# Kernel tuning notes

Hardware: AMD Instinct MI355X
Metric: run time of the kernel (lower is better)

Reference implementation:

```python
import jax, jax.numpy as jnp
import numpy as np

D = 256
H = 4
L = 6
N = 32768
NH = N // H  # 8192 per-head width
VOCAB = 256
B, T = 1, 1024
ROPE_BASE = 10000.0


def ln(x):
    # LayerNorm over last dim, no affine (elementwise_affine=False)
    m = jnp.mean(x, axis=-1, keepdims=True)
    v = jnp.var(x, axis=-1, keepdims=True)
    return (x - m) * jax.lax.rsqrt(v + 1e-5)


def rope(x):
    # standard rotary position embedding over the last dim (split-half convention)
    Dh = x.shape[-1]
    t = x.shape[-2]
    half = Dh // 2
    inv_freq = 1.0 / (ROPE_BASE ** (jnp.arange(half, dtype=jnp.float32) / half))
    ang = jnp.arange(t, dtype=jnp.float32)[:, None] * inv_freq[None, :]  # [T, half]
    cos, sin = jnp.cos(ang), jnp.sin(ang)
    x1, x2 = x[..., :half], x[..., half:]
    return jnp.concatenate([x1 * cos - x2 * sin, x2 * cos + x1 * sin], axis=-1)


def setup_inputs() -> dict:
    key = jax.random.key(0)
    ks = jax.random.split(key, 6)
    std = 0.02
    return {
        "idx": jax.random.randint(ks[0], (B, T), 0, VOCAB, dtype=jnp.int32),
        "wte": std * jax.random.normal(ks[1], (VOCAB, D), dtype=jnp.float32),
        "encoder": std * jax.random.normal(ks[2], (N, D), dtype=jnp.float32),
        "decoder_x": std * jax.random.normal(ks[3], (H, D, NH), dtype=jnp.float32),
        "decoder_y": std * jax.random.normal(ks[4], (H, D, NH), dtype=jnp.float32),
        "readout": std * jax.random.normal(ks[5], (D, VOCAB), dtype=jnp.float32),
    }


def reference(idx, wte, encoder, decoder_x, decoder_y, readout):
    b, t = idx.shape
    v = ln(wte[idx])  # [B, T, D]
    # strict causal mask (tril with diagonal=-1): position i attends to j < i
    mask = jnp.tril(jnp.ones((t, t), dtype=bool), k=-1)
    for _ in range(L):
        # x: relu(v @ decoder_x) -> [B, H, T, NH]
        x = jax.nn.relu(jnp.einsum('btd,hdn->bhtn', v, decoder_x))
        xr = rope(x)  # Q = K = x
        # unnormalized causal linear attention, strict lower triangular
        scores = jnp.einsum('bhtn,bhsn->bhts', xr, xr)
        scores = jnp.where(mask, scores, 0.0)
        a = jnp.einsum('bhts,bsd->bhtd', scores, v)  # V = v (broadcast over heads)
        # gated wide projection
        y = jax.nn.relu(jnp.einsum('bhtd,hdn->bhtn', ln(a), decoder_y)) * x
        # [B,H,T,NH] -> [B,T,H*NH] = [B,T,N]  (matches transpose(1,2).reshape)
        y = jnp.transpose(y, (0, 2, 1, 3)).reshape(b, t, N)
        v = ln(v + ln(y @ encoder))  # dropout is identity in eval
    return v @ readout  # [B, T, VOCAB]
```

## Files before the change

kernel.cpp:

```cpp
#include <hip/hip_runtime.h>
#include <hip/hip_bf16.h>
#include <stdint.h>

typedef unsigned short u16;
typedef unsigned int u32;
typedef __attribute__((ext_vector_type(8))) short i16x8;
typedef __attribute__((ext_vector_type(4))) float f32x4;

#define DEV __device__ __forceinline__

constexpr int T = 1024, D = 256, H = 4, NH = 8192, NF = 32768, HALF = 4096;

constexpr size_t OFF_DXT  = 0;
constexpr size_t OFF_DYT  = OFF_DXT  + (size_t)H*NH*D*2;
constexpr size_t OFF_ENCT = OFF_DYT  + (size_t)H*NH*D*2;
constexpr size_t OFF_ROT  = OFF_ENCT + (size_t)D*NF*2;
constexpr size_t OFF_COS  = OFF_ROT  + (size_t)D*D*2;
constexpr size_t OFF_SIN  = OFF_COS  + (size_t)T*HALF*4;
constexpr size_t OFF_V    = OFF_SIN  + (size_t)T*HALF*4;
constexpr size_t OFF_VBF  = OFF_V    + (size_t)T*D*4;
constexpr size_t OFF_VT   = OFF_VBF  + (size_t)T*D*2;
constexpr size_t OFF_X    = OFF_VT   + (size_t)T*D*2;
constexpr size_t OFF_XR   = OFF_X    + (size_t)T*NF*2;
constexpr size_t OFF_SC   = OFF_XR   + (size_t)T*NF*2;
constexpr size_t OFF_LA   = OFF_SC   + (size_t)H*T*T*2;
constexpr size_t OFF_PART = OFF_LA   + (size_t)H*T*D*2;
constexpr size_t WS_NEED  = OFF_PART + (size_t)8*T*T*4;


DEV u16 f2bf(float f) {
  u32 u = __float_as_uint(f);
  u += 0x7FFFu + ((u >> 16) & 1u);
  return (u16)(u >> 16);
}
DEV float bf2f(u16 u) { return __uint_as_float(((u32)u) << 16); }

DEV float2 block_sum2(float a, float b, float* sb) {
  #pragma unroll
  for (int o = 32; o > 0; o >>= 1) {
    a += __shfl_down(a, o, 64);
    b += __shfl_down(b, o, 64);
  }
  const int w = threadIdx.x >> 6;
  __syncthreads();
  if ((threadIdx.x & 63) == 0) { sb[w*2] = a; sb[w*2+1] = b; }
  __syncthreads();
  return make_float2(sb[0]+sb[2]+sb[4]+sb[6], sb[1]+sb[3]+sb[5]+sb[7]);
}

DEV void stage128(const u16* __restrict__ g, int ld, char* lds, int wave, int lane) {
  #pragma unroll
  for (int i = 0; i < 4; ++i) {
    const int f = (wave*4 + i)*64 + lane;
    const int row = f >> 3, seg = f & 7;
    const int segl = seg ^ (row & 7);
    const u16* src = g + (size_t)row*ld + segl*8;
    __builtin_amdgcn_global_load_lds(
        (const __attribute__((address_space(1))) void*)src,
        (__attribute__((address_space(3))) void*)(lds + ((wave*4 + i) << 10)),
        16, 0, 0);
  }
}

DEV void gemm_bt_core(const u16* __restrict__ Ab, int lda,
                      const u16* __restrict__ Bb, int ldb,
                      int nkt, char* smem, f32x4 acc[4][4]) {
  const int tid = threadIdx.x, lane = tid & 63, wave = tid >> 6;
  const int wm = wave >> 1, wn = wave & 1;
  const int lr = lane & 15, lk = lane >> 4;
  char* As = smem;
  char* Bs = smem + 32768;
  #pragma unroll
  for (int m = 0; m < 4; ++m)
    #pragma unroll
    for (int n = 0; n < 4; ++n) acc[m][n] = f32x4{0.f, 0.f, 0.f, 0.f};
  stage128(Ab, lda, As, wave, lane);
  stage128(Bb, ldb, Bs, wave, lane);
  __syncthreads();
  for (int kt = 0; kt < nkt; ++kt) {
    const int cur = kt & 1;
    if (kt + 1 < nkt) {
      stage128(Ab + (size_t)(kt+1)*64, lda, As + ((cur^1) << 14), wave, lane);
      stage128(Bb + (size_t)(kt+1)*64, ldb, Bs + ((cur^1) << 14), wave, lane);
    }
    const char* Ac = As + (cur << 14);
    const char* Bc = Bs + (cur << 14);
    #pragma unroll
    for (int kk = 0; kk < 2; ++kk) {
      const int lcol = kk*64 + lk*16;
      i16x8 af[4], bfv[4];
      #pragma unroll
      for (int m = 0; m < 4; ++m) {
        const int row = wm*64 + m*16 + lr;
        af[m] = *(const i16x8*)(Ac + row*128 + (lcol ^ ((row & 7) << 4)));
      }
      #pragma unroll
      for (int n = 0; n < 4; ++n) {
        const int row = wn*64 + n*16 + lr;
        bfv[n] = *(const i16x8*)(Bc + row*128 + (lcol ^ ((row & 7) << 4)));
      }
      #pragma unroll
      for (int m = 0; m < 4; ++m)
        #pragma unroll
        for (int n = 0; n < 4; ++n)
          acc[m][n] = __builtin_amdgcn_mfma_f32_16x16x32_bf16(af[m], bfv[n], acc[m][n], 0, 0, 0);
    }
    __syncthreads();
  }
}

#define EPILOG_IDX() \
  const int lane = threadIdx.x & 63, wave = threadIdx.x >> 6; \
  const int wm = wave >> 1, wn = wave & 1, lr = lane & 15, lk = lane >> 4; \
  const int r0 = wm*64 + lk*4; \
  const int c0 = wn*64 + lr;

constexpr int TS = 136;
template<int MODE>
DEV void store_tile(const f32x4 acc[4][4], u16* __restrict__ dst, int ld,
                    const u16* __restrict__ xg, char* smem) {
  u16* tb = (u16*)smem;
  EPILOG_IDX();
  #pragma unroll
  for (int m = 0; m < 4; ++m)
    #pragma unroll
    for (int n = 0; n < 4; ++n)
      #pragma unroll
      for (int r = 0; r < 4; ++r) {
        float v = acc[m][n][r];
        if (MODE >= 1) v = fmaxf(v, 0.f);
        tb[(size_t)(r0 + m*16 + r)*TS + c0 + n*16] = f2bf(v);
      }
  __syncthreads();
  const int rr = threadIdx.x >> 4;
  const int cc = (threadIdx.x & 15)*8;
  #pragma unroll
  for (int it = 0; it < 8; ++it) {
    const int row = it*16 + rr;
    i16x8 w = *(const i16x8*)(tb + (size_t)row*TS + cc);
    if (MODE == 2) {
      const i16x8 xv = *(const i16x8*)(xg + (size_t)row*ld + cc);
      #pragma unroll
      for (int j = 0; j < 8; ++j)
        w[j] = (short)f2bf(bf2f((u16)w[j]) * bf2f((u16)xv[j]));
    }
    *(i16x8*)(dst + (size_t)row*ld + cc) = w;
  }
}

template<int PERM>
__global__ __launch_bounds__(256) void k_transpose_cvt(const float* __restrict__ in,
                                                       u16* __restrict__ out, int R, int C) {
  __shared__ float tile[32][33];
  const size_t zoff = (size_t)blockIdx.z * R * C;
  const float* inz = in + zoff;
  u16* outz = out + zoff;
  const int c0 = blockIdx.x << 5, rr0 = blockIdx.y << 5;
  const int tx = threadIdx.x & 31, ty = threadIdx.x >> 5;
  #pragma unroll
  for (int i = 0; i < 4; ++i) {
    int irow = rr0 + ty + i*8;
    if (PERM == 2) {
      const int hh = irow >> 13, j = irow & 8191;
      irow = hh*8192 + ((j & 1) ? (j >> 1) + 4096 : (j >> 1));
    }
    tile[ty + i*8][tx] = inz[(size_t)irow*C + c0 + tx];
  }
  __syncthreads();
  #pragma unroll
  for (int i = 0; i < 4; ++i) {
    const int rr = ty + i*8;
    int orow = c0 + rr;
    if (PERM == 1) {
      const int j = orow & 8191;
      orow = (orow & ~8191) | ((j < 4096) ? 2*j : 2*(j - 4096) + 1);
    }
    outz[(size_t)orow*R + rr0 + tx] = f2bf(tile[tx][rr]);
  }
}

__global__ __launch_bounds__(256) void k_rope_table(float* __restrict__ cosT,
                                                    float* __restrict__ sinT) {
  const int i = blockIdx.x*256 + threadIdx.x;
  const int t = blockIdx.y;
  const float p = (float)i * (1.f/4096.f);
  const float ang = (float)t * expf(-9.210340371976184f * p);
  cosT[(size_t)t*HALF + i] = cosf(ang);
  sinT[(size_t)t*HALF + i] = sinf(ang);
}

__global__ __launch_bounds__(256) void k_embed(const int* __restrict__ idx,
                                               const float* __restrict__ wte,
                                               float* __restrict__ v,
                                               u16* __restrict__ vbf, u16* __restrict__ vT) {
  __shared__ float sb[8];
  const int t = blockIdx.x, d = threadIdx.x;
  const float val = wte[(size_t)idx[t]*D + d];
  float2 ss = block_sum2(val, val*val, sb);
  const float m = ss.x*(1.f/256.f), var = ss.y*(1.f/256.f) - m*m;
  const float vn = (val - m) * rsqrtf(var + 1e-5f);
  v[(size_t)t*D + d] = vn;
  const u16 b = f2bf(vn);
  vbf[(size_t)t*D + d] = b;
  vT[(size_t)d*T + t] = b;
}

__global__ __launch_bounds__(256) void k_gemm_x_rope(const u16* __restrict__ vbf,
                                                     const u16* __restrict__ dxT,
                                                     u16* __restrict__ x,
                                                     u16* __restrict__ xr,
                                                     const float* __restrict__ cosT,
                                                     const float* __restrict__ sinT) {
  __shared__ char smem[65536];
  const int nt = blockIdx.x, mt = blockIdx.y, h = blockIdx.z;
  f32x4 acc[4][4];
  gemm_bt_core(vbf + (size_t)mt*128*D, D,
               dxT + ((size_t)h*NH + (size_t)nt*128)*D, D, 4, smem, acc);
  u16* tb = (u16*)smem;
  {
    EPILOG_IDX();
    #pragma unroll
    for (int m = 0; m < 4; ++m)
      #pragma unroll
      for (int n = 0; n < 4; ++n)
        #pragma unroll
        for (int r = 0; r < 4; ++r)
          tb[(size_t)(r0 + m*16 + r)*TS + c0 + n*16] = f2bf(fmaxf(acc[m][n][r], 0.f));
  }
  __syncthreads();
  const int rr = threadIdx.x >> 4;
  const int cc = (threadIdx.x & 15)*8;
  const size_t obase = (size_t)mt*128*NF + (size_t)h*NH + (size_t)nt*128;
  const int pbase = (nt*128 + cc) >> 1;
  #pragma unroll
  for (int it = 0; it < 8; ++it) {
    const int row = it*16 + rr;
    const i16x8 w = *(const i16x8*)(tb + (size_t)row*TS + cc);
    *(i16x8*)(x + obase + (size_t)row*NF + cc) = w;
    const int t = mt*128 + row;
    const float4 cv = *(const float4*)(cosT + (size_t)t*HALF + pbase);
    const float4 sv = *(const float4*)(sinT + (size_t)t*HALF + pbase);
    i16x8 r;
    float x1, x2;
    x1 = bf2f((u16)w[0]); x2 = bf2f((u16)w[1]);
    r[0] = (short)f2bf(x1*cv.x - x2*sv.x); r[1] = (short)f2bf(x2*cv.x + x1*sv.x);
    x1 = bf2f((u16)w[2]); x2 = bf2f((u16)w[3]);
    r[2] = (short)f2bf(x1*cv.y - x2*sv.y); r[3] = (short)f2bf(x2*cv.y + x1*sv.y);
    x1 = bf2f((u16)w[4]); x2 = bf2f((u16)w[5]);
    r[4] = (short)f2bf(x1*cv.z - x2*sv.z); r[5] = (short)f2bf(x2*cv.z + x1*sv.z);
    x1 = bf2f((u16)w[6]); x2 = bf2f((u16)w[7]);
    r[6] = (short)f2bf(x1*cv.w - x2*sv.w); r[7] = (short)f2bf(x2*cv.w + x1*sv.w);
    *(i16x8*)(xr + obase + (size_t)row*NF + cc) = r;
  }
}

__global__ __launch_bounds__(256) void k_gemm_sc(const u16* __restrict__ xr,
                                                 u16* __restrict__ scb) {
  __shared__ char smem[65536];
  const int z = blockIdx.x & 15;
  const int i = blockIdx.x >> 4;
  int tt = 0;
  while ((tt + 1)*(tt + 2)/2 <= i) ++tt;
  const int st = i - tt*(tt + 1)/2;
  const int h = z >> 2, kc = z & 3;
  const u16* base = xr + (size_t)h*NH + (size_t)kc*2048;
  f32x4 acc[4][4];
  gemm_bt_core(base + (size_t)tt*128*NF, NF, base + (size_t)st*128*NF, NF, 32, smem, acc);
  store_tile<0>(acc, scb + (size_t)z*T*T + (size_t)tt*128*T + (size_t)st*128, T,
                nullptr, smem);
}

__global__ __launch_bounds__(256) void k_sc_combine(const u16* __restrict__ scb,
                                                    u16* __restrict__ sc) {
  const int row = blockIdx.x;
  const int h = row >> 10, t = row & 1023;
  const u16* p0 = scb + ((size_t)(h*4 + 0)*T + t)*T;
  u16* o = sc + (size_t)row*T;
  const int s0 = threadIdx.x*4;
  ushort4 r;
  if (s0 >= t) {
    r.x = 0; r.y = 0; r.z = 0; r.w = 0;
  } else {
    const ushort4 a0 = *(const ushort4*)(p0 + s0);
    const ushort4 a1 = *(const ushort4*)(p0 + T*T + s0);
    const ushort4 a2 = *(const ushort4*)(p0 + 2*(size_t)T*T + s0);
    const ushort4 a3 = *(const ushort4*)(p0 + 3*(size_t)T*T + s0);
    const float vx = bf2f(a0.x) + bf2f(a1.x) + bf2f(a2.x) + bf2f(a3.x);
    const float vy = bf2f(a0.y) + bf2f(a1.y) + bf2f(a2.y) + bf2f(a3.y);
    const float vz = bf2f(a0.z) + bf2f(a1.z) + bf2f(a2.z) + bf2f(a3.z);
    const float vw = bf2f(a0.w) + bf2f(a1.w) + bf2f(a2.w) + bf2f(a3.w);
    r.x = f2bf((s0 + 0 < t) ? vx : 0.f);
    r.y = f2bf((s0 + 1 < t) ? vy : 0.f);
    r.z = f2bf((s0 + 2 < t) ? vz : 0.f);
    r.w = f2bf((s0 + 3 < t) ? vw : 0.f);
  }
  *(ushort4*)(o + s0) = r;
}

__global__ __launch_bounds__(256) void k_gemm_av(const u16* __restrict__ sc,
                                                 const u16* __restrict__ vT,
                                                 float* __restrict__ part) {
  __shared__ char smem[65536];
  const int slot = blockIdx.x & 7;
  const int h = slot >> 1, nt = slot & 1;
  int mt = 0, kc = 0, rem = blockIdx.x >> 3;
  #pragma unroll
  for (int m = 0; m < 8; ++m) {
    const int c = (m >> 1) + 1;
    if (rem < c) { mt = m; kc = rem; break; }
    rem -= c;
  }
  f32x4 acc[4][4];
  gemm_bt_core(sc + ((size_t)h*T + (size_t)mt*128)*T + (size_t)kc*256, T,
               vT + (size_t)nt*128*T + (size_t)kc*256, T, 4, smem, acc);
  EPILOG_IDX();
  float* Cp = part + (size_t)(h*4 + kc) * T * D;
  const int tb = mt*128 + r0, cb = nt*128 + c0;
  #pragma unroll
  for (int m = 0; m < 4; ++m)
    #pragma unroll
    for (int n = 0; n < 4; ++n)
      #pragma unroll
      for (int r = 0; r < 4; ++r)
        Cp[(size_t)(tb + m*16 + r)*D + cb + n*16] = acc[m][n][r];
}

__global__ __launch_bounds__(256) void k_ln_a(const float* __restrict__ part,
                                              u16* __restrict__ la) {
  __shared__ float sb[8];
  const int row = blockIdx.x;
  const int h = row >> 10, t = row & 1023;
  const int d = threadIdx.x;
  const int nkc = ((t >> 7) >> 1) + 1;
  float s = 0.f;
  for (int kc = 0; kc < nkc; ++kc)
    s += part[((size_t)(h*4 + kc)*T + t)*D + d];
  float2 ss = block_sum2(s, s*s, sb);
  const float m = ss.x*(1.f/256.f), var = ss.y*(1.f/256.f) - m*m;
  la[(size_t)row*D + d] = f2bf((s - m) * rsqrtf(var + 1e-5f));
}

__global__ __launch_bounds__(256) void k_gemm_y(const u16* __restrict__ la,
                                                const u16* __restrict__ dyT,
                                                const u16* __restrict__ x,
                                                u16* __restrict__ y) {
  __shared__ char smem[65536];
  const int nt = blockIdx.x, mt = blockIdx.y, h = blockIdx.z;
  f32x4 acc[4][4];
  gemm_bt_core(la + ((size_t)h*T + (size_t)mt*128)*D, D,
               dyT + ((size_t)h*NH + (size_t)nt*128)*D, D, 4, smem, acc);
  const size_t off = (size_t)mt*128*NF + (size_t)h*NH + (size_t)nt*128;
  store_tile<2>(acc, y + off, NF, x + off, smem);
}

__global__ __launch_bounds__(256) void k_gemm_enc(const u16* __restrict__ y,
                                                  const u16* __restrict__ encT,
                                                  float* __restrict__ part) {
  __shared__ char smem[65536];
  const int slot = blockIdx.x & 7;
  const int seq  = blockIdx.x >> 3;
  const int kcc = slot*4 + (seq >> 4);
  const int nt = seq & 1;
  const int mt = (seq >> 1) & 7;
  f32x4 acc[4][4];
  gemm_bt_core(y + (size_t)mt*128*NF + (size_t)kcc*1024, NF,
               encT + (size_t)nt*128*NF + (size_t)kcc*1024, NF, 16, smem, acc);
  EPILOG_IDX();
  float* Cp = part + (size_t)kcc * T * D;
  const int tb = mt*128 + r0, cb = nt*128 + c0;
  #pragma unroll
  for (int m = 0; m < 4; ++m)
    #pragma unroll
    for (int n = 0; n < 4; ++n)
      #pragma unroll
      for (int r = 0; r < 4; ++r)
        Cp[(size_t)(tb + m*16 + r)*D + cb + n*16] = acc[m][n][r];
}

__global__ __launch_bounds__(256) void k_newv(const float* __restrict__ part,
                                              float* __restrict__ v,
                                              u16* __restrict__ vbf, u16* __restrict__ vT) {
  __shared__ float sb[8];
  const int t = blockIdx.x, d = threadIdx.x;
  float s = 0.f;
  #pragma unroll
  for (int kc = 0; kc < 32; ++kc)
    s += part[((size_t)kc*T + t)*D + d];
  float2 ss = block_sum2(s, s*s, sb);
  float m = ss.x*(1.f/256.f), var = ss.y*(1.f/256.f) - m*m;
  const float l1 = (s - m) * rsqrtf(var + 1e-5f);
  const float u = v[(size_t)t*D + d] + l1;
  float2 s2 = block_sum2(u, u*u, sb);
  m = s2.x*(1.f/256.f); var = s2.y*(1.f/256.f) - m*m;
  const float vn = (u - m) * rsqrtf(var + 1e-5f);
  v[(size_t)t*D + d] = vn;
  const u16 bb = f2bf(vn);
  vbf[(size_t)t*D + d] = bb;
  vT[(size_t)d*T + t] = bb;
}

__global__ __launch_bounds__(256) void k_gemm_out(const u16* __restrict__ vbf,
                                                  const u16* __restrict__ roT,
                                                  float* __restrict__ out) {
  __shared__ char smem[65536];
  const int nt = blockIdx.x, mt = blockIdx.y;
  f32x4 acc[4][4];
  gemm_bt_core(vbf + (size_t)mt*128*D, D, roT + (size_t)nt*128*D, D, 4, smem, acc);
  EPILOG_IDX();
  const int tb = mt*128 + r0, cb = nt*128 + c0;
  #pragma unroll
  for (int m = 0; m < 4; ++m)
    #pragma unroll
    for (int n = 0; n < 4; ++n)
      #pragma unroll
      for (int r = 0; r < 4; ++r)
        out[(size_t)(tb + m*16 + r)*D + cb + n*16] = acc[m][n][r];
}

extern "C" void kernel_launch(void* const* d_in, const int* in_sizes, int n_in,
                              void* d_out, int out_size, void* d_ws, size_t ws_size,
                              hipStream_t stream) {
  (void)in_sizes; (void)n_in; (void)out_size; (void)ws_size;
  const int*   idx = (const int*)d_in[0];
  const float* wte = (const float*)d_in[1];
  const float* enc = (const float*)d_in[2];
  const float* dx  = (const float*)d_in[3];
  const float* dy  = (const float*)d_in[4];
  const float* ro  = (const float*)d_in[5];
  float* out = (float*)d_out;
  char* ws = (char*)d_ws;

  u16* dxT  = (u16*)(ws + OFF_DXT);
  u16* dyT  = (u16*)(ws + OFF_DYT);
  u16* encT = (u16*)(ws + OFF_ENCT);
  u16* roT  = (u16*)(ws + OFF_ROT);
  float* cosT = (float*)(ws + OFF_COS);
  float* sinT = (float*)(ws + OFF_SIN);
  float* v    = (float*)(ws + OFF_V);
  u16* vbf  = (u16*)(ws + OFF_VBF);
  u16* vT   = (u16*)(ws + OFF_VT);
  u16* x    = (u16*)(ws + OFF_X);
  u16* xr   = (u16*)(ws + OFF_XR);
  u16* sc   = (u16*)(ws + OFF_SC);
  u16* la   = (u16*)(ws + OFF_LA);
  u16* scb  = (u16*)(ws + OFF_PART);
  float* part = (float*)(ws + OFF_PART);

  k_transpose_cvt<1><<<dim3(NH/32, D/32, H), 256, 0, stream>>>(dx, dxT, D, NH);
  k_transpose_cvt<1><<<dim3(NH/32, D/32, H), 256, 0, stream>>>(dy, dyT, D, NH);
  k_transpose_cvt<2><<<dim3(D/32, NF/32, 1), 256, 0, stream>>>(enc, encT, NF, D);
  k_transpose_cvt<0><<<dim3(D/32, D/32, 1), 256, 0, stream>>>(ro, roT, D, D);
  k_rope_table<<<dim3(HALF/256, T), 256, 0, stream>>>(cosT, sinT);
  k_embed<<<T, 256, 0, stream>>>(idx, wte, v, vbf, vT);

  for (int l = 0; l < 6; ++l) {
    k_gemm_x_rope<<<dim3(64, 8, H), 256, 0, stream>>>(vbf, dxT, x, xr, cosT, sinT);
    k_gemm_sc <<<576,              256, 0, stream>>>(xr, scb);
    k_sc_combine<<<H*T,            256, 0, stream>>>(scb, sc);
    k_gemm_av <<<160,              256, 0, stream>>>(sc, vT, part);
    k_ln_a    <<<H*T,              256, 0, stream>>>(part, la);
    k_gemm_y  <<<dim3(64, 8, H),   256, 0, stream>>>(la, dyT, x, xr );
    k_gemm_enc<<<512,              256, 0, stream>>>(xr , encT, part);
    k_newv    <<<T,                256, 0, stream>>>(part, v, vbf, vT);
  }
  k_gemm_out<<<dim3(2, 8), 256, 0, stream>>>(vbf, roT, out);
}
```

Measured before the change: 1.273 ms.

## Use single-buffered 32KB LDS GEMM and split epilogue to raise occupancy

The x/rope and y GEMM kernels (K=256, only 4 k-steps) now use a single-buffered LDS staging loop and a two-pass epilogue that writes half the tile at a time. This halves shared memory to 32KB, and launch bounds of 5 blocks per CU are added so more workgroups can be resident and hide memory latency. In exchange there is no intra-block prefetch overlap and there are extra barriers in both the main loop and the epilogue.

```diff
diff --git a/kernel.cpp b/kernel.cpp
--- a/kernel.cpp
+++ b/kernel.cpp
@@ -62,6 +62,30 @@
   }
 }
 
+DEV void mfma_tile(const char* Ac, const char* Bc, int wm, int wn, int lr, int lk,
+                   f32x4 acc[4][4]) {
+  #pragma unroll
+  for (int kk = 0; kk < 2; ++kk) {
+    const int lcol = kk*64 + lk*16;
+    i16x8 af[4], bfv[4];
+    #pragma unroll
+    for (int m = 0; m < 4; ++m) {
+      const int row = wm*64 + m*16 + lr;
+      af[m] = *(const i16x8*)(Ac + row*128 + (lcol ^ ((row & 7) << 4)));
+    }
+    #pragma unroll
+    for (int n = 0; n < 4; ++n) {
+      const int row = wn*64 + n*16 + lr;
+      bfv[n] = *(const i16x8*)(Bc + row*128 + (lcol ^ ((row & 7) << 4)));
+    }
+    #pragma unroll
+    for (int m = 0; m < 4; ++m)
+      #pragma unroll
+      for (int n = 0; n < 4; ++n)
+        acc[m][n] = __builtin_amdgcn_mfma_f32_16x16x32_bf16(af[m], bfv[n], acc[m][n], 0, 0, 0);
+  }
+}
+
 DEV void gemm_bt_core(const u16* __restrict__ Ab, int lda,
                       const u16* __restrict__ Bb, int ldb,
                       int nkt, char* smem, f32x4 acc[4][4]) {
@@ -83,28 +107,28 @@
       stage128(Ab + (size_t)(kt+1)*64, lda, As + ((cur^1) << 14), wave, lane);
       stage128(Bb + (size_t)(kt+1)*64, ldb, Bs + ((cur^1) << 14), wave, lane);
     }
-    const char* Ac = As + (cur << 14);
-    const char* Bc = Bs + (cur << 14);
-    #pragma unroll
-    for (int kk = 0; kk < 2; ++kk) {
-      const int lcol = kk*64 + lk*16;
-      i16x8 af[4], bfv[4];
-      #pragma unroll
-      for (int m = 0; m < 4; ++m) {
-        const int row = wm*64 + m*16 + lr;
-        af[m] = *(const i16x8*)(Ac + row*128 + (lcol ^ ((row & 7) << 4)));
-      }
-      #pragma unroll
-      for (int n = 0; n < 4; ++n) {
-        const int row = wn*64 + n*16 + lr;
-        bfv[n] = *(const i16x8*)(Bc + row*128 + (lcol ^ ((row & 7) << 4)));
-      }
-      #pragma unroll
-      for (int m = 0; m < 4; ++m)
-        #pragma unroll
-        for (int n = 0; n < 4; ++n)
-          acc[m][n] = __builtin_amdgcn_mfma_f32_16x16x32_bf16(af[m], bfv[n], acc[m][n], 0, 0, 0);
-    }
+    mfma_tile(As + (cur << 14), Bs + (cur << 14), wm, wn, lr, lk, acc);
+    __syncthreads();
+  }
+}
+
+DEV void gemm_bt_core_sb(const u16* __restrict__ Ab, int lda,
+                         const u16* __restrict__ Bb, int ldb,
+                         int nkt, char* smem, f32x4 acc[4][4]) {
+  const int tid = threadIdx.x, lane = tid & 63, wave = tid >> 6;
+  const int wm = wave >> 1, wn = wave & 1;
+  const int lr = lane & 15, lk = lane >> 4;
+  char* As = smem;
+  char* Bs = smem + 16384;
+  #pragma unroll
+  for (int m = 0; m < 4; ++m)
+    #pragma unroll
+    for (int n = 0; n < 4; ++n) acc[m][n] = f32x4{0.f, 0.f, 0.f, 0.f};
+  for (int kt = 0; kt < nkt; ++kt) {
+    stage128(Ab + (size_t)kt*64, lda, As, wave, lane);
+    stage128(Bb + (size_t)kt*64, ldb, Bs, wave, lane);
+    __syncthreads();
+    mfma_tile(As, Bs, wm, wn, lr, lk, acc);
     __syncthreads();
   }
 }
@@ -116,6 +140,7 @@
   const int c0 = wn*64 + lr;
 
 constexpr int TS = 136;
+
 template<int MODE>
 DEV void store_tile(const f32x4 acc[4][4], u16* __restrict__ dst, int ld,
                     const u16* __restrict__ xg, char* smem) {
@@ -145,6 +170,46 @@
         w[j] = (short)f2bf(bf2f((u16)w[j]) * bf2f((u16)xv[j]));
     }
     *(i16x8*)(dst + (size_t)row*ld + cc) = w;
+  }
+}
+
+template<int MODE>
+DEV void store_tile_sb(const f32x4 acc[4][4], u16* __restrict__ dst, int ld,
+                       const u16* __restrict__ xg, char* smem) {
+  u16* tb = (u16*)smem;
+  const int lane = threadIdx.x & 63, wave = threadIdx.x >> 6;
+  const int wm = wave >> 1, wn = wave & 1, lr = lane & 15, lk = lane >> 4;
+  const int c0 = wn*64 + lr, rb = lk*4;
+  const int rr = threadIdx.x >> 4, cc = (threadIdx.x & 15)*8;
+  #pragma unroll
+  for (int half = 0; half < 2; ++half) {
+    if (wm == half) {
+      #pragma unroll
+      for (int m = 0; m < 4; ++m)
+        #pragma unroll
+        for (int n = 0; n < 4; ++n)
+          #pragma unroll
+          for (int r = 0; r < 4; ++r) {
+            float v = acc[m][n][r];
+            if (MODE >= 1) v = fmaxf(v, 0.f);
+            tb[(size_t)(rb + m*16 + r)*TS + c0 + n*16] = f2bf(v);
+          }
+    }
+    __syncthreads();
+    #pragma unroll
+    for (int it = 0; it < 4; ++it) {
+      const int row = it*16 + rr;
+      const int grow = half*64 + row;
+      i16x8 w = *(const i16x8*)(tb + (size_t)row*TS + cc);
+      if (MODE == 2) {
+        const i16x8 xv = *(const i16x8*)(xg + (size_t)grow*ld + cc);
+        #pragma unroll
+        for (int j = 0; j < 8; ++j)
+          w[j] = (short)f2bf(bf2f((u16)w[j]) * bf2f((u16)xv[j]));
+      }
+      *(i16x8*)(dst + (size_t)grow*ld + cc) = w;
+    }
+    __syncthreads();
   }
 }
 
@@ -205,52 +270,58 @@
   vT[(size_t)d*T + t] = b;
 }
 
-__global__ __launch_bounds__(256) void k_gemm_x_rope(const u16* __restrict__ vbf,
-                                                     const u16* __restrict__ dxT,
-                                                     u16* __restrict__ x,
-                                                     u16* __restrict__ xr,
-                                                     const float* __restrict__ cosT,
-                                                     const float* __restrict__ sinT) {
-  __shared__ char smem[65536];
+__global__ __launch_bounds__(256, 5) void k_gemm_x_rope(const u16* __restrict__ vbf,
+                                                        const u16* __restrict__ dxT,
+                                                        u16* __restrict__ x,
+                                                        u16* __restrict__ xr,
+                                                        const float* __restrict__ cosT,
+                                                        const float* __restrict__ sinT) {
+  __shared__ char smem[32768];
   const int nt = blockIdx.x, mt = blockIdx.y, h = blockIdx.z;
   f32x4 acc[4][4];
-  gemm_bt_core(vbf + (size_t)mt*128*D, D,
-               dxT + ((size_t)h*NH + (size_t)nt*128)*D, D, 4, smem, acc);
+  gemm_bt_core_sb(vbf + (size_t)mt*128*D, D,
+                  dxT + ((size_t)h*NH + (size_t)nt*128)*D, D, 4, smem, acc);
   u16* tb = (u16*)smem;
-  {
-    EPILOG_IDX();
-    #pragma unroll
-    for (int m = 0; m < 4; ++m)
-      #pragma unroll
-      for (int n = 0; n < 4; ++n)
-        #pragma unroll
-        for (int r = 0; r < 4; ++r)
-          tb[(size_t)(r0 + m*16 + r)*TS + c0 + n*16] = f2bf(fmaxf(acc[m][n][r], 0.f));
-  }
-  __syncthreads();
-  const int rr = threadIdx.x >> 4;
-  const int cc = (threadIdx.x & 15)*8;
+  const int lane = threadIdx.x & 63, wave = threadIdx.x >> 6;
+  const int wm = wave >> 1, wn = wave & 1, lr = lane & 15, lk = lane >> 4;
+  const int c0 = wn*64 + lr, rb = lk*4;
+  const int rr = threadIdx.x >> 4, cc = (threadIdx.x & 15)*8;
   const size_t obase = (size_t)mt*128*NF + (size_t)h*NH + (size_t)nt*128;
   const int pbase = (nt*128 + cc) >> 1;
   #pragma unroll
-  for (int it = 0; it < 8; ++it) {
-    const int row = it*16 + rr;
-    const i16x8 w = *(const i16x8*)(tb + (size_t)row*TS + cc);
-    *(i16x8*)(x + obase + (size_t)row*NF + cc) = w;
-    const int t = mt*128 + row;
-    const float4 cv = *(const float4*)(cosT + (size_t)t*HALF + pbase);
-    const float4 sv = *(const float4*)(sinT + (size_t)t*HALF + pbase);
-    i16x8 r;
-    float x1, x2;
-    x1 = bf2f((u16)w[0]); x2 = bf2f((u16)w[1]);
-    r[0] = (short)f2bf(x1*cv.x - x2*sv.x); r[1] = (short)f2bf(x2*cv.x + x1*sv.x);
-    x1 = bf2f((u16)w[2]); x2 = bf2f((u16)w[3]);
-    r[2] = (short)f2bf(x1*cv.y - x2*sv.y); r[3] = (short)f2bf(x2*cv.y + x1*sv.y);
-    x1 = bf2f((u16)w[4]); x2 = bf2f((u16)w[5]);
-    r[4] = (short)f2bf(x1*cv.z - x2*sv.z); r[5] = (short)f2bf(x2*cv.z + x1*sv.z);
-    x1 = bf2f((u16)w[6]); x2 = bf2f((u16)w[7]);
-    r[6] = (short)f2bf(x1*cv.w - x2*sv.w); r[7] = (short)f2bf(x2*cv.w + x1*sv.w);
-    *(i16x8*)(xr + obase + (size_t)row*NF + cc) = r;
+  for (int half = 0; half < 2; ++half) {
+    if (wm == half) {
+      #pragma unroll
+      for (int m = 0; m < 4; ++m)
+        #pragma unroll
+        for (int n = 0; n < 4; ++n)
+          #pragma unroll
+          for (int r = 0; r < 4; ++r)
+            tb[(size_t)(rb + m*16 + r)*TS + c0 + n*16] = f2bf(fmaxf(acc[m][n][r], 0.f));
+    }
+    __syncthreads();
+    #pragma unroll
+    for (int it = 0; it < 4; ++it) {
+      const int row = it*16 + rr;
+      const int grow = half*64 + row;
+      const i16x8 w = *(const i16x8*)(tb + (size_t)row*TS + cc);
+      *(i16x8*)(x + obase + (size_t)grow*NF + cc) = w;
+      const int t = mt*128 + grow;
+      const float4 cv = *(const float4*)(cosT + (size_t)t*HALF + pbase);
+      const float4 sv = *(const float4*)(sinT + (size_t)t*HALF + pbase);
+      i16x8 rg;
+      float x1, x2;
+      x1 = bf2f((u16)w[0]); x2 = bf2f((u16)w[1]);
+      rg[0] = (short)f2bf(x1*cv.x - x2*sv.x); rg[1] = (short)f2bf(x2*cv.x + x1*sv.x);
+      x1 = bf2f((u16)w[2]); x2 = bf2f((u16)w[3]);
+      rg[2] = (short)f2bf(x1*cv.y - x2*sv.y); rg[3] = (short)f2bf(x2*cv.y + x1*sv.y);
+      x1 = bf2f((u16)w[4]); x2 = bf2f((u16)w[5]);
+      rg[4] = (short)f2bf(x1*cv.z - x2*sv.z); rg[5] = (short)f2bf(x2*cv.z + x1*sv.z);
+      x1 = bf2f((u16)w[6]); x2 = bf2f((u16)w[7]);
+      rg[6] = (short)f2bf(x1*cv.w - x2*sv.w); rg[7] = (short)f2bf(x2*cv.w + x1*sv.w);
+      *(i16x8*)(xr + obase + (size_t)grow*NF + cc) = rg;
+    }
+    __syncthreads();
   }
 }
 
@@ -340,17 +411,17 @@
   la[(size_t)row*D + d] = f2bf((s - m) * rsqrtf(var + 1e-5f));
 }
 
-__global__ __launch_bounds__(256) void k_gemm_y(const u16* __restrict__ la,
-                                                const u16* __restrict__ dyT,
-                                                const u16* __restrict__ x,
-                                                u16* __restrict__ y) {
-  __shared__ char smem[65536];
+__global__ __launch_bounds__(256, 5) void k_gemm_y(const u16* __restrict__ la,
+                                                   const u16* __restrict__ dyT,
+                                                   const u16* __restrict__ x,
+                                                   u16* __restrict__ y) {
+  __shared__ char smem[32768];
   const int nt = blockIdx.x, mt = blockIdx.y, h = blockIdx.z;
   f32x4 acc[4][4];
-  gemm_bt_core(la + ((size_t)h*T + (size_t)mt*128)*D, D,
-               dyT + ((size_t)h*NH + (size_t)nt*128)*D, D, 4, smem, acc);
+  gemm_bt_core_sb(la + ((size_t)h*T + (size_t)mt*128)*D, D,
+                  dyT + ((size_t)h*NH + (size_t)nt*128)*D, D, 4, smem, acc);
   const size_t off = (size_t)mt*128*NF + (size_t)h*NH + (size_t)nt*128;
-  store_tile<2>(acc, y + off, NF, x + off, smem);
+  store_tile_sb<2>(acc, y + off, NF, x + off, smem);
 }
 
 __global__ __launch_bounds__(256) void k_gemm_enc(const u16* __restrict__ y,
```

Result: slower. 1.959 ms (+53.9%).
